# Optimization experiments

Hardware: AMD Instinct MI355X
Metric: run time of the kernel (lower is better)

Reference implementation:

```python
import jax, jax.numpy as jnp
import numpy as np

N_NODES = 100_000
N_EDGES = 1_600_000
N_TRI = 1_000_000
HID = 64
NNZ0 = 2 * N_EDGES  # d0: 2 nonzeros per edge
NNZ1 = 3 * N_TRI    # d1: 3 nonzeros per 2-clique


def spmm(rows, cols, vals, x, n_out):
    """out[r] = sum_{k: rows[k]==r} vals[k] * x[cols[k]]  (sparse @ dense)."""
    return jax.ops.segment_sum(vals[:, None] * x[cols], rows, num_segments=n_out)


def setup_inputs() -> dict:
    key = jax.random.key(0)
    ks = jax.random.split(key, 12)
    q = jax.random.normal(ks[0], (N_NODES, HID), dtype=jnp.float32)
    p = jax.random.normal(ks[1], (N_EDGES, HID), dtype=jnp.float32)
    # attention weights used as divisors -> keep bounded away from 0
    A0 = jax.random.uniform(ks[2], (N_NODES,), jnp.float32, 0.5, 1.5)
    A1 = jax.random.uniform(ks[3], (N_EDGES,), jnp.float32, 0.5, 1.5)
    A2 = jax.random.uniform(ks[4], (N_TRI,), jnp.float32, 0.5, 1.5)
    alpha_raw = jnp.ones((1,), dtype=jnp.float32)
    d0_rows = jax.random.randint(ks[5], (NNZ0,), 0, N_EDGES, dtype=jnp.int32)
    d0_cols = jax.random.randint(ks[6], (NNZ0,), 0, N_NODES, dtype=jnp.int32)
    d0_vals = jax.random.normal(ks[7], (NNZ0,), dtype=jnp.float32)
    d1_rows = jax.random.randint(ks[8], (NNZ1,), 0, N_TRI, dtype=jnp.int32)
    d1_cols = jax.random.randint(ks[9], (NNZ1,), 0, N_EDGES, dtype=jnp.int32)
    d1_vals = jax.random.normal(ks[10], (NNZ1,), dtype=jnp.float32)
    return {
        "q": q, "p": p, "A0": A0, "A1": A1, "A2": A2, "alpha_raw": alpha_raw,
        "d0_rows": d0_rows, "d0_cols": d0_cols, "d0_vals": d0_vals,
        "d1_rows": d1_rows, "d1_cols": d1_cols, "d1_vals": d1_vals,
    }


def reference(q, p, A0, A1, A2, alpha_raw,
              d0_rows, d0_cols, d0_vals, d1_rows, d1_cols, d1_vals):
    n_nodes = q.shape[0]
    n_edges = p.shape[0]
    n_tri = A2.shape[0]
    alpha = jax.nn.sigmoid(alpha_raw)  # opt['alpha_multiplier']
    a0 = A0[:, None]  # [N,1]
    a1 = A1[:, None]  # [E,1]
    a2 = A2[:, None]  # [T,1]

    # bracket == 'gradient'
    # qPart = -alpha * d0^T (A1 * d0 (q / A0)) / A0
    d0ainvq = spmm(d0_rows, d0_cols, d0_vals, q / a0, n_edges)          # [E,H]
    qPart = -alpha * spmm(d0_cols, d0_rows, d0_vals, a1 * d0ainvq, n_nodes) / a0

    # pPart = -alpha * ( d1^T (A2 * d1 (p / A1)) / A1 + d0 (d0^T p / A0) )
    d1ainvp = spmm(d1_rows, d1_cols, d1_vals, p / a1, n_tri)            # [T,H]
    d1ad1Part = spmm(d1_cols, d1_rows, d1_vals, a2 * d1ainvp, n_edges) / a1
    a0invd0tp = spmm(d0_cols, d0_rows, d0_vals, p, n_nodes) / a0        # [N,H]
    d0d0aPart = spmm(d0_rows, d0_cols, d0_vals, a0invd0tp, n_edges)     # [E,H]
    pPart = -alpha * (d1ad1Part + d0d0aPart)

    return (qPart, pPart)
```

## Files before the change

kernel.cpp:

```cpp
#include <hip/hip_runtime.h>

#define HID 64

typedef unsigned short ushort_t;
typedef unsigned int uint_t;
typedef float fx4 __attribute__((ext_vector_type(4)));

__device__ __forceinline__ ushort_t f2bf(float f) {
    uint_t u = __float_as_uint(f);
    u += 0x7FFFu + ((u >> 16) & 1u);
    return (ushort_t)(u >> 16);
}
__device__ __forceinline__ float bf2f(ushort_t h) {
    return __uint_as_float(((uint_t)h) << 16);
}

__device__ __forceinline__ void ntstore4(float* dst, float a, float b, float c, float d) {
    fx4 t; t[0] = a; t[1] = b; t[2] = c; t[3] = d;
    __builtin_nontemporal_store(t, (fx4*)dst);
}


__global__ __launch_bounds__(256) void count_pair(const int* __restrict__ ra,
                                                  const int* __restrict__ rb,
                                                  int* __restrict__ rowcat,
                                                  int offa, int offb, int nnz) {
    int k = blockIdx.x * 256 + threadIdx.x;
    if (k >= nnz) return;
    atomicAdd(&rowcat[offa + ra[k] + 1], 1);
    atomicAdd(&rowcat[offb + rb[k] + 1], 1);
}

__global__ __launch_bounds__(256) void fill_pair(const int* __restrict__ ra,
                                                 const int* __restrict__ rb,
                                                 const float* __restrict__ vals,
                                                 const float* __restrict__ divdiag,
                                                 int* __restrict__ rowcat,
                                                 int offa, int offb,
                                                 int2* __restrict__ pcvcat, int nnz) {
    int k = blockIdx.x * 256 + threadIdx.x;
    if (k >= nnz) return;
    int A = __builtin_nontemporal_load(ra + k);
    int B = __builtin_nontemporal_load(rb + k);
    float v = __builtin_nontemporal_load(vals + k);
    float vd = v / divdiag[B];
    int pa = atomicAdd(&rowcat[offa + A], 1);
    int2 e1; e1.x = B; e1.y = __float_as_int(vd);
    pcvcat[pa] = e1;
    int pb = atomicAdd(&rowcat[offb + B], 1);
    int2 e2; e2.x = A; e2.y = __float_as_int(v);
    pcvcat[pb] = e2;
}

#define SCAN_TPB 256
#define SCAN_IPT 32
#define SCAN_TILE (SCAN_TPB * SCAN_IPT)

__global__ __launch_bounds__(256) void scan1(int* __restrict__ data,
                                             int* __restrict__ blockSums, int n) {
    __shared__ int sdata[SCAN_TPB];
    int base = blockIdx.x * SCAN_TILE + threadIdx.x * SCAN_IPT;
    int v[SCAN_IPT];
    int s = 0;
#pragma unroll
    for (int i = 0; i < SCAN_IPT; ++i) {
        int idx = base + i;
        int x = (idx < n) ? data[idx] : 0;
        s += x;
        v[i] = s;
    }
    sdata[threadIdx.x] = s;
    __syncthreads();
    for (int off = 1; off < SCAN_TPB; off <<= 1) {
        int t = (threadIdx.x >= off) ? sdata[threadIdx.x - off] : 0;
        __syncthreads();
        sdata[threadIdx.x] += t;
        __syncthreads();
    }
    int excl = (threadIdx.x == 0) ? 0 : sdata[threadIdx.x - 1];
#pragma unroll
    for (int i = 0; i < SCAN_IPT; ++i) {
        int idx = base + i;
        if (idx < n) data[idx] = v[i] + excl;
    }
    if (threadIdx.x == SCAN_TPB - 1) blockSums[blockIdx.x] = sdata[SCAN_TPB - 1];
}

__global__ __launch_bounds__(1024) void scan2(int* __restrict__ blockSums, int nb) {
    __shared__ int sdata[1024];
    int x = (threadIdx.x < nb) ? blockSums[threadIdx.x] : 0;
    sdata[threadIdx.x] = x;
    __syncthreads();
    for (int off = 1; off < 1024; off <<= 1) {
        int t = (threadIdx.x >= off) ? sdata[threadIdx.x - off] : 0;
        __syncthreads();
        sdata[threadIdx.x] += t;
        __syncthreads();
    }
    if (threadIdx.x < nb) blockSums[threadIdx.x] = sdata[threadIdx.x];
}

__global__ __launch_bounds__(256) void scan3(int* __restrict__ data,
                                             const int* __restrict__ blockSums, int n) {
    if (blockIdx.x == 0) return;
    int add = blockSums[blockIdx.x - 1];
    int base = blockIdx.x * SCAN_TILE + threadIdx.x;
#pragma unroll
    for (int i = 0; i < SCAN_IPT; ++i) {
        int idx = base + i * SCAN_TPB;
        if (idx < n) data[idx] += add;
    }
}


__global__ __launch_bounds__(256) void f32_to_bf16(const float* __restrict__ src,
                                                   ushort_t* __restrict__ dst, size_t n) {
    size_t i = ((size_t)blockIdx.x * 256 + threadIdx.x) * 4;
    if (i + 3 < n) {
        float4 v = *(const float4*)(src + i);
        ushort4 o;
        o.x = f2bf(v.x); o.y = f2bf(v.y); o.z = f2bf(v.z); o.w = f2bf(v.w);
        *(ushort4*)(dst + i) = o;
    } else {
        for (; i < n; ++i) dst[i] = f2bf(src[i]);
    }
}


template <int SRCH>
__device__ __forceinline__ float4 gather_row(const void* __restrict__ xv, int col, int h4) {
    if constexpr (SRCH) {
        ushort4 hv = *((const ushort4*)((const ushort_t*)xv + (size_t)col * HID) + h4);
        float4 r; r.x = bf2f(hv.x); r.y = bf2f(hv.y); r.z = bf2f(hv.z); r.w = bf2f(hv.w);
        return r;
    } else {
        return *((const float4*)((const float*)xv + (size_t)col * HID) + h4);
    }
}

template <int SRCH, int OUTH>
__global__ __launch_bounds__(256) void csr_spmm4(
    const int* __restrict__ rps, const int2* __restrict__ pcv,
    const void* __restrict__ xv, void* __restrict__ outv,
    const float* __restrict__ rmul, const float* __restrict__ rdiv,
    const float* __restrict__ alpha_raw, int nrows)
{
    int h4 = threadIdx.x & 15;
    int sub16 = threadIdx.x >> 4;
    int rbase = (blockIdx.x * 16 + sub16) * 4;
    if (rbase >= nrows) return;
    int rp[5];
#pragma unroll
    for (int i = 0; i < 5; ++i) rp[i] = rps[min(rbase + i, nrows)];
    int len[4];
#pragma unroll
    for (int r = 0; r < 4; ++r) len[r] = rp[r + 1] - rp[r];
    int maxlen = max(max(len[0], len[1]), max(len[2], len[3]));
    float4 acc[4];
#pragma unroll
    for (int r = 0; r < 4; ++r) acc[r] = float4{0.f, 0.f, 0.f, 0.f};

    for (int j = 0; j < maxlen; ++j) {
#pragma unroll
        for (int r = 0; r < 4; ++r) {
            if (j < len[r]) {
                int2 e = pcv[rp[r] + j];
                float v = __int_as_float(e.y);
                float4 g = gather_row<SRCH>(xv, e.x, h4);
                acc[r].x += v * g.x; acc[r].y += v * g.y;
                acc[r].z += v * g.z; acc[r].w += v * g.w;
            }
        }
    }

    float sgn = alpha_raw ? -(1.0f / (1.0f + expf(-alpha_raw[0]))) : 1.0f;
#pragma unroll
    for (int r = 0; r < 4; ++r) {
        int row = rbase + r;
        if (row >= nrows) break;
        float s = sgn;
        if (rmul) s *= rmul[row];
        if (rdiv) s /= rdiv[row];
        float4 a = acc[r];
        a.x *= s; a.y *= s; a.z *= s; a.w *= s;
        if constexpr (OUTH) {
            ushort4 o;
            o.x = f2bf(a.x); o.y = f2bf(a.y); o.z = f2bf(a.z); o.w = f2bf(a.w);
            *((ushort4*)((ushort_t*)outv + (size_t)row * HID) + h4) = o;
        } else {
            ntstore4((float*)((float4*)((float*)outv + (size_t)row * HID) + h4),
                     a.x, a.y, a.z, a.w);
        }
    }
}

__global__ __launch_bounds__(256) void csr_fused4(
    const int* __restrict__ rpsA, const int* __restrict__ rpsB,
    const int2* __restrict__ pcv,
    const ushort_t* __restrict__ xA, const ushort_t* __restrict__ xB,
    const float* __restrict__ a1d, const float* __restrict__ alpha_raw,
    float* __restrict__ out, int nrows)
{
    int h4 = threadIdx.x & 15;
    int sub16 = threadIdx.x >> 4;
    int rbase = (blockIdx.x * 16 + sub16) * 4;
    if (rbase >= nrows) return;

    int rpA[5], rpB[5];
#pragma unroll
    for (int i = 0; i < 5; ++i) {
        int idx = min(rbase + i, nrows);
        rpA[i] = rpsA[idx];
        rpB[i] = rpsB[idx];
    }
    int lA[4], lB[4];
#pragma unroll
    for (int r = 0; r < 4; ++r) { lA[r] = rpA[r+1] - rpA[r]; lB[r] = rpB[r+1] - rpB[r]; }
    int mA = max(max(lA[0], lA[1]), max(lA[2], lA[3]));
    int mB = max(max(lB[0], lB[1]), max(lB[2], lB[3]));

    float4 accA[4], accB[4];
#pragma unroll
    for (int r = 0; r < 4; ++r) { accA[r] = float4{0,0,0,0}; accB[r] = float4{0,0,0,0}; }

    for (int j = 0; j < mA; ++j) {
#pragma unroll
        for (int r = 0; r < 4; ++r) {
            if (j < lA[r]) {
                int2 e = pcv[rpA[r] + j];
                float v = __int_as_float(e.y);
                ushort4 hv = *((const ushort4*)(xA + (size_t)e.x * HID) + h4);
                accA[r].x += v * bf2f(hv.x); accA[r].y += v * bf2f(hv.y);
                accA[r].z += v * bf2f(hv.z); accA[r].w += v * bf2f(hv.w);
            }
        }
    }
    for (int j = 0; j < mB; ++j) {
#pragma unroll
        for (int r = 0; r < 4; ++r) {
            if (j < lB[r]) {
                int2 e = pcv[rpB[r] + j];
                float v = __int_as_float(e.y);
                ushort4 hv = *((const ushort4*)(xB + (size_t)e.x * HID) + h4);
                accB[r].x += v * bf2f(hv.x); accB[r].y += v * bf2f(hv.y);
                accB[r].z += v * bf2f(hv.z); accB[r].w += v * bf2f(hv.w);
            }
        }
    }

    float ns = -(1.0f / (1.0f + expf(-alpha_raw[0])));
#pragma unroll
    for (int r = 0; r < 4; ++r) {
        int row = rbase + r;
        if (row >= nrows) break;
        float inv_a1 = 1.0f / a1d[row];
        ntstore4((float*)((float4*)(out + (size_t)row * HID) + h4),
                 ns * (accA[r].x + accB[r].x * inv_a1),
                 ns * (accA[r].y + accB[r].y * inv_a1),
                 ns * (accA[r].z + accB[r].z * inv_a1),
                 ns * (accA[r].w + accB[r].w * inv_a1));
    }
}


__global__ __launch_bounds__(256) void count_rows(const int* __restrict__ ridx,
                                                  int* __restrict__ rowptr, int nnz) {
    int k = blockIdx.x * 256 + threadIdx.x;
    if (k < nnz) atomicAdd(&rowptr[ridx[k] + 1], 1);
}

__global__ __launch_bounds__(256) void copy_int(const int* __restrict__ src,
                                                int* __restrict__ dst, int n) {
    int i = blockIdx.x * 256 + threadIdx.x;
    if (i < n) dst[i] = src[i];
}

__global__ __launch_bounds__(256) void fill_csr(const int* __restrict__ ridx,
                                                const int* __restrict__ cidx,
                                                const float* __restrict__ vals,
                                                int* __restrict__ cursor,
                                                int2* __restrict__ pcv, int nnz) {
    int k = blockIdx.x * 256 + threadIdx.x;
    if (k >= nnz) return;
    int pos = atomicAdd(&cursor[ridx[k]], 1);
    int2 e;
    e.x = cidx[k];
    e.y = __float_as_int(vals[k]);
    pcv[pos] = e;
}

template <int SRCH, int OUTH>
__global__ __launch_bounds__(256) void csr_spmm_t(
    const int* __restrict__ rowptr, const int2* __restrict__ pcv,
    const void* __restrict__ xv, void* __restrict__ outv,
    const float* __restrict__ gdiag, int gdiv,
    const float* __restrict__ rmul,
    const float* __restrict__ rdiv,
    const float* __restrict__ alpha_raw,
    int nrows)
{
    int lane = threadIdx.x & 63;
    int wave = threadIdx.x >> 6;
    int sub = lane >> 4;
    int h4 = lane & 15;
    int row = blockIdx.x * 16 + wave * 4 + sub;
    if (row >= nrows) return;
    int start = rowptr[row], end = rowptr[row + 1];
    float4 acc = {0.f, 0.f, 0.f, 0.f};
    for (int j = start; j < end; ++j) {
        int2 e = pcv[j];
        int c = e.x;
        float v = __int_as_float(e.y);
        if (gdiag) { float t = gdiag[c]; v = gdiv ? v / t : v * t; }
        float4 xvv = gather_row<SRCH>(xv, c, h4);
        acc.x += v * xvv.x; acc.y += v * xvv.y; acc.z += v * xvv.z; acc.w += v * xvv.w;
    }
    float s = 1.0f;
    if (rmul) s *= rmul[row];
    if (rdiv) s /= rdiv[row];
    if (alpha_raw) s *= -(1.0f / (1.0f + expf(-alpha_raw[0])));
    acc.x *= s; acc.y *= s; acc.z *= s; acc.w *= s;
    if constexpr (OUTH) {
        ushort_t* out = (ushort_t*)outv;
        ushort4 o;
        o.x = f2bf(acc.x); o.y = f2bf(acc.y); o.z = f2bf(acc.z); o.w = f2bf(acc.w);
        *((ushort4*)(out + (size_t)row * HID) + h4) = o;
    } else {
        float* out = (float*)outv;
        *((float4*)(out + (size_t)row * HID) + h4) = acc;
    }
}

template <int BH>
__global__ __launch_bounds__(256) void csr_spmm_fused_t(
    const int* __restrict__ rowptrA, const int2* __restrict__ pcvA, const float* __restrict__ xA,
    const int* __restrict__ rowptrB, const int2* __restrict__ pcvB, const void* __restrict__ xBv,
    const float* __restrict__ a1, const float* __restrict__ alpha_raw,
    float* __restrict__ out, int nrows)
{
    int lane = threadIdx.x & 63;
    int wave = threadIdx.x >> 6;
    int sub = lane >> 4;
    int h4 = lane & 15;
    int row = blockIdx.x * 16 + wave * 4 + sub;
    if (row >= nrows) return;

    float4 accA = {0.f, 0.f, 0.f, 0.f};
    {
        int start = rowptrA[row], end = rowptrA[row + 1];
        for (int j = start; j < end; ++j) {
            int2 e = pcvA[j];
            float v = __int_as_float(e.y);
            const float4 xv = *((const float4*)(xA + (size_t)e.x * HID) + h4);
            accA.x += v * xv.x; accA.y += v * xv.y; accA.z += v * xv.z; accA.w += v * xv.w;
        }
    }
    float4 accB = {0.f, 0.f, 0.f, 0.f};
    {
        int start = rowptrB[row], end = rowptrB[row + 1];
        for (int j = start; j < end; ++j) {
            int2 e = pcvB[j];
            float v = __int_as_float(e.y);
            float4 xv = gather_row<BH>(xBv, e.x, h4);
            accB.x += v * xv.x; accB.y += v * xv.y; accB.z += v * xv.z; accB.w += v * xv.w;
        }
    }
    float inv_a1 = 1.0f / a1[row];
    float ns = -(1.0f / (1.0f + expf(-alpha_raw[0])));
    float4 r;
    r.x = ns * (accA.x + accB.x * inv_a1);
    r.y = ns * (accA.y + accB.y * inv_a1);
    r.z = ns * (accA.z + accB.z * inv_a1);
    r.w = ns * (accA.w + accB.w * inv_a1);
    *((float4*)(out + (size_t)row * HID) + h4) = r;
}

__global__ __launch_bounds__(256) void spmm_scatter(
    const int* __restrict__ gidx, const int* __restrict__ sidx,
    const float* __restrict__ vals, const float* __restrict__ x,
    float* __restrict__ out,
    const float* __restrict__ gscale, int ginv,
    const float* __restrict__ sscale, int sinv,
    const float* __restrict__ alpha_raw, int nnz)
{
    int k = (blockIdx.x << 2) | (threadIdx.x >> 6);
    if (k >= nnz) return;
    int h = threadIdx.x & 63;
    int g = gidx[k];
    int s = sidx[k];
    float f = vals[k];
    if (gscale) { float t = gscale[g]; f = ginv ? (f / t) : (f * t); }
    if (sscale) { float t = sscale[s]; f = sinv ? (f / t) : (f * t); }
    if (alpha_raw) {
        float sig = 1.0f / (1.0f + expf(-alpha_raw[0]));
        f = -f * sig;
    }
    atomicAdd(out + (size_t)s * HID + h, f * x[(size_t)g * HID + h]);
}


extern "C" void kernel_launch(void* const* d_in, const int* in_sizes, int n_in,
                              void* d_out, int out_size, void* d_ws, size_t ws_size,
                              hipStream_t stream) {
    const float* q         = (const float*)d_in[0];
    const float* p         = (const float*)d_in[1];
    const float* A0        = (const float*)d_in[2];
    const float* A1        = (const float*)d_in[3];
    const float* A2        = (const float*)d_in[4];
    const float* alpha_raw = (const float*)d_in[5];
    const int*   d0_rows   = (const int*)d_in[6];
    const int*   d0_cols   = (const int*)d_in[7];
    const float* d0_vals   = (const float*)d_in[8];
    const int*   d1_rows   = (const int*)d_in[9];
    const int*   d1_cols   = (const int*)d_in[10];
    const float* d1_vals   = (const float*)d_in[11];

    const int n_nodes = in_sizes[2];
    const int n_edges = in_sizes[3];
    const int n_tri   = in_sizes[4];
    const int nnz0    = in_sizes[6];
    const int nnz1    = in_sizes[9];

    float* qPart = (float*)d_out;
    float* pPart = (float*)d_out + (size_t)n_nodes * HID;

    const size_t qPartBytes = (size_t)n_nodes * HID * sizeof(float);
    const size_t pPartBytes = (size_t)n_edges * HID * sizeof(float);

    dim3 blk(256);

    const int off_d0r = 0;
    const int off_d0c = off_d0r + n_edges;
    const int off_d1r = off_d0c + n_nodes;
    const int off_d1c = off_d1r + n_tri;
    const int NR      = off_d1c + n_edges;

    {
        char* w = (char*)d_ws;
        auto alloc = [&](size_t bytes) -> char* {
            char* ptr = w;
            w += (bytes + 255) & ~(size_t)255;
            return ptr;
        };
        ushort_t* bufA   = (ushort_t*)alloc((size_t)n_edges * HID * sizeof(ushort_t));
        ushort_t* tmp_th = (ushort_t*)alloc((size_t)n_tri * HID * sizeof(ushort_t));
        ushort_t* tmp_nh = (ushort_t*)alloc((size_t)n_nodes * HID * sizeof(ushort_t));
        int*      Z      = (int*)alloc((size_t)(NR + 2) * sizeof(int));
        int*      rowcat = Z + 1;
        int*      blockSums = (int*)alloc(2048 * sizeof(int));
        int2*     pcvcat = (int2*)alloc(((size_t)nnz0 * 2 + (size_t)nnz1 * 2) * sizeof(int2));
        size_t needed = (size_t)(w - (char*)d_ws);

        if (needed <= ws_size) {
            hipMemsetAsync(Z, 0, (size_t)(NR + 2) * sizeof(int), stream);
            dim3 gk0((nnz0 + 255) / 256);
            dim3 gk1((nnz1 + 255) / 256);
            count_pair<<<gk0, blk, 0, stream>>>(d0_rows, d0_cols, rowcat, off_d0r, off_d0c, nnz0);
            count_pair<<<gk1, blk, 0, stream>>>(d1_rows, d1_cols, rowcat, off_d1r, off_d1c, nnz1);
            {
                int n = NR + 1;
                int nb = (n + SCAN_TILE - 1) / SCAN_TILE;
                scan1<<<nb, SCAN_TPB, 0, stream>>>(rowcat, blockSums, n);
                scan2<<<1, 1024, 0, stream>>>(blockSums, nb);
                scan3<<<nb, SCAN_TPB, 0, stream>>>(rowcat, blockSums, n);
            }
            fill_pair<<<gk0, blk, 0, stream>>>(d0_rows, d0_cols, d0_vals, A0,
                                               rowcat, off_d0r, off_d0c, pcvcat, nnz0);
            fill_pair<<<gk1, blk, 0, stream>>>(d1_rows, d1_cols, d1_vals, A1,
                                               rowcat, off_d1r, off_d1c, pcvcat, nnz1);

            size_t np = (size_t)n_edges * HID;
            f32_to_bf16<<<(unsigned)((np / 4 + 255) / 256), blk, 0, stream>>>(p, bufA, np);

            csr_spmm4<1, 1><<<(n_tri + 63) / 64, blk, 0, stream>>>(
                Z + off_d1r, pcvcat, bufA, tmp_th, A2, nullptr, nullptr, n_tri);

            csr_spmm4<1, 1><<<(n_nodes + 63) / 64, blk, 0, stream>>>(
                Z + off_d0c, pcvcat, bufA, tmp_nh, nullptr, nullptr, nullptr, n_nodes);

            csr_spmm4<0, 1><<<(n_edges + 63) / 64, blk, 0, stream>>>(
                Z + off_d0r, pcvcat, q, bufA, A1, nullptr, nullptr, n_edges);

            csr_spmm4<1, 0><<<(n_nodes + 63) / 64, blk, 0, stream>>>(
                Z + off_d0c, pcvcat, bufA, qPart, nullptr, A0, alpha_raw, n_nodes);

            csr_fused4<<<(n_edges + 63) / 64, blk, 0, stream>>>(
                Z + off_d0r, Z + off_d1c, pcvcat, tmp_nh, tmp_th,
                A1, alpha_raw, pPart, n_edges);
            return;
        }
    }

    {
        char* w = (char*)d_ws;
        auto alloc = [&](size_t bytes) -> char* {
            char* ptr = w;
            w += (bytes + 255) & ~(size_t)255;
            return ptr;
        };
        float* tmp_t = (float*)alloc((size_t)n_tri * HID * sizeof(float));
        float* tmp_n = (float*)alloc((size_t)n_nodes * HID * sizeof(float));
        size_t rpTotal = (size_t)(n_edges + 1) + (n_nodes + 1) + (n_tri + 1) + (n_edges + 1);
        int* rpBase = (int*)alloc(rpTotal * sizeof(int));
        int* rp_d0r = rpBase;
        int* rp_d0c = rp_d0r + (n_edges + 1);
        int* rp_d1r = rp_d0c + (n_nodes + 1);
        int* rp_d1c = rp_d1r + (n_tri + 1);
        int nmax = n_edges > n_tri ? n_edges : n_tri;
        if (n_nodes > nmax) nmax = n_nodes;
        int* cursor    = (int*)alloc((size_t)nmax * sizeof(int));
        int* blockSums = (int*)alloc(2048 * sizeof(int));
        int2* pcv_d0r = (int2*)alloc((size_t)nnz0 * sizeof(int2));
        int2* pcv_d0c = (int2*)alloc((size_t)nnz0 * sizeof(int2));
        int2* pcv_d1r = (int2*)alloc((size_t)nnz1 * sizeof(int2));
        int2* pcv_d1c = (int2*)alloc((size_t)nnz1 * sizeof(int2));
        size_t needed = (size_t)(w - (char*)d_ws);

        if (needed <= ws_size) {
            hipMemsetAsync(rpBase, 0, rpTotal * sizeof(int), stream);
            dim3 gk0((nnz0 + 255) / 256);
            dim3 gk1((nnz1 + 255) / 256);
            count_rows<<<gk0, blk, 0, stream>>>(d0_rows, rp_d0r, nnz0);
            count_rows<<<gk0, blk, 0, stream>>>(d0_cols, rp_d0c, nnz0);
            count_rows<<<gk1, blk, 0, stream>>>(d1_rows, rp_d1r, nnz1);
            count_rows<<<gk1, blk, 0, stream>>>(d1_cols, rp_d1c, nnz1);

            struct Build {
                int* rowptr; int nout; const int* ridx; const int* cidx; const float* vals;
                int2* pcv; int nnz;
            } builds[4] = {
                { rp_d0r, n_edges, d0_rows, d0_cols, d0_vals, pcv_d0r, nnz0 },
                { rp_d0c, n_nodes, d0_cols, d0_rows, d0_vals, pcv_d0c, nnz0 },
                { rp_d1r, n_tri,   d1_rows, d1_cols, d1_vals, pcv_d1r, nnz1 },
                { rp_d1c, n_edges, d1_cols, d1_rows, d1_vals, pcv_d1c, nnz1 },
            };
            for (int b = 0; b < 4; ++b) {
                int n = builds[b].nout + 1;
                int nb = (n + SCAN_TILE - 1) / SCAN_TILE;
                scan1<<<nb, SCAN_TPB, 0, stream>>>(builds[b].rowptr, blockSums, n);
                scan2<<<1, 1024, 0, stream>>>(blockSums, nb);
                scan3<<<nb, SCAN_TPB, 0, stream>>>(builds[b].rowptr, blockSums, n);
                copy_int<<<(builds[b].nout + 255) / 256, blk, 0, stream>>>(
                    builds[b].rowptr, cursor, builds[b].nout);
                fill_csr<<<(builds[b].nnz + 255) / 256, blk, 0, stream>>>(
                    builds[b].ridx, builds[b].cidx, builds[b].vals, cursor,
                    builds[b].pcv, builds[b].nnz);
            }

            float* tmp_e1 = pPart;
            csr_spmm_t<0, 0><<<(n_edges + 15) / 16, blk, 0, stream>>>(
                rp_d0r, pcv_d0r, q, tmp_e1, A0, 1, A1, nullptr, nullptr, n_edges);
            csr_spmm_t<0, 0><<<(n_nodes + 15) / 16, blk, 0, stream>>>(
                rp_d0c, pcv_d0c, tmp_e1, qPart, nullptr, 0, nullptr, A0, alpha_raw, n_nodes);
            csr_spmm_t<0, 0><<<(n_tri + 15) / 16, blk, 0, stream>>>(
                rp_d1r, pcv_d1r, p, tmp_t, A1, 1, A2, nullptr, nullptr, n_tri);
            csr_spmm_t<0, 0><<<(n_nodes + 15) / 16, blk, 0, stream>>>(
                rp_d0c, pcv_d0c, p, tmp_n, nullptr, 0, nullptr, A0, nullptr, n_nodes);
            csr_spmm_fused_t<0><<<(n_edges + 15) / 16, blk, 0, stream>>>(
                rp_d0r, pcv_d0r, tmp_n,
                rp_d1c, pcv_d1c, tmp_t,
                A1, alpha_raw, pPart, n_edges);
            return;
        }
    }

    {
        float* tmp = (float*)d_ws;
        const size_t triBytes  = (size_t)n_tri * HID * sizeof(float);
        const size_t nodeBytes = qPartBytes;
        dim3 g0((nnz0 + 3) / 4);
        dim3 g1((nnz1 + 3) / 4);
        hipMemsetAsync(qPart, 0, qPartBytes, stream);
        hipMemsetAsync(pPart, 0, pPartBytes, stream);
        spmm_scatter<<<g0, blk, 0, stream>>>(d0_cols, d0_rows, d0_vals, q, pPart,
                                             A0, 1, nullptr, 0, nullptr, nnz0);
        spmm_scatter<<<g0, blk, 0, stream>>>(d0_rows, d0_cols, d0_vals, pPart, qPart,
                                             A1, 0, A0, 1, alpha_raw, nnz0);
        hipMemsetAsync(pPart, 0, pPartBytes, stream);
        hipMemsetAsync(tmp, 0, triBytes, stream);
        spmm_scatter<<<g1, blk, 0, stream>>>(d1_cols, d1_rows, d1_vals, p, tmp,
                                             A1, 1, nullptr, 0, nullptr, nnz1);
        spmm_scatter<<<g1, blk, 0, stream>>>(d1_rows, d1_cols, d1_vals, tmp, pPart,
                                             A2, 0, A1, 1, alpha_raw, nnz1);
        hipMemsetAsync(tmp, 0, nodeBytes, stream);
        spmm_scatter<<<g0, blk, 0, stream>>>(d0_rows, d0_cols, d0_vals, p, tmp,
                                             nullptr, 0, A0, 1, nullptr, nnz0);
        spmm_scatter<<<g0, blk, 0, stream>>>(d0_cols, d0_rows, d0_vals, tmp, pPart,
                                             nullptr, 0, nullptr, 0, alpha_raw, nnz0);
    }
}
```

Baseline: 2.375 ms.

## Fuse CSR build passes and spmm stages, record atomic ranks to drop fill atomics

The count pass now records each nonzero's rank from the atomic counter, so the fill pass can place entries without a second round of atomics. The fill pass is merged with the fp32-to-bf16 conversion of p, with fill and convert blocks interleaved. The two spmm stages that read p are merged into one launch. The q-path edge spmm is fused into the final pPart kernel because both walk the same d0-row CSR. Gather loops are unrolled by two with clamped indices so loads are issued early. Ranks are stored as 16-bit values, which assumes no row has more than 65535 entries, and the rank buffer reuses tmp_th.

```diff
diff --git a/kernel.cpp b/kernel.cpp
--- a/kernel.cpp
+++ b/kernel.cpp
@@ -4,6 +4,7 @@
 
 typedef unsigned short ushort_t;
 typedef unsigned int uint_t;
+typedef unsigned long long ull_t;
 typedef float fx4 __attribute__((ext_vector_type(4)));
 
 __device__ __forceinline__ ushort_t f2bf(float f) {
@@ -20,36 +21,106 @@
     __builtin_nontemporal_store(t, (fx4*)dst);
 }
 
-
-__global__ __launch_bounds__(256) void count_pair(const int* __restrict__ ra,
-                                                  const int* __restrict__ rb,
-                                                  int* __restrict__ rowcat,
-                                                  int offa, int offb, int nnz) {
-    int k = blockIdx.x * 256 + threadIdx.x;
-    if (k >= nnz) return;
-    atomicAdd(&rowcat[offa + ra[k] + 1], 1);
-    atomicAdd(&rowcat[offb + rb[k] + 1], 1);
-}
-
-__global__ __launch_bounds__(256) void fill_pair(const int* __restrict__ ra,
-                                                 const int* __restrict__ rb,
-                                                 const float* __restrict__ vals,
-                                                 const float* __restrict__ divdiag,
-                                                 int* __restrict__ rowcat,
-                                                 int offa, int offb,
-                                                 int2* __restrict__ pcvcat, int nnz) {
-    int k = blockIdx.x * 256 + threadIdx.x;
-    if (k >= nnz) return;
-    int A = __builtin_nontemporal_load(ra + k);
-    int B = __builtin_nontemporal_load(rb + k);
-    float v = __builtin_nontemporal_load(vals + k);
-    float vd = v / divdiag[B];
-    int pa = atomicAdd(&rowcat[offa + A], 1);
-    int2 e1; e1.x = B; e1.y = __float_as_int(vd);
-    pcvcat[pa] = e1;
-    int pb = atomicAdd(&rowcat[offb + B], 1);
-    int2 e2; e2.x = A; e2.y = __float_as_int(v);
-    pcvcat[pb] = e2;
+__device__ __forceinline__ ull_t packCV(int col, float v) {
+    return ((ull_t)(uint_t)__float_as_int(v) << 32) | (uint_t)col;
+}
+
+
+__global__ __launch_bounds__(256) void count_rank2(
+    const int* __restrict__ d0r, const int* __restrict__ d0c,
+    const int* __restrict__ d1r, const int* __restrict__ d1c,
+    int* __restrict__ rowcat,
+    ushort2* __restrict__ rank0, ushort2* __restrict__ rank1,
+    int off_d0r, int off_d0c, int off_d1r, int off_d1c,
+    int nnz0, int nnz1)
+{
+    int b = blockIdx.x;
+    int cb0 = (nnz0 + 255) >> 8;
+    if (b < cb0) {
+        int k = b * 256 + threadIdx.x;
+        if (k < nnz0) {
+            int A = d0r[k], B = d0c[k];
+            int r0 = atomicAdd(&rowcat[off_d0r + A + 1], 1);
+            int r1 = atomicAdd(&rowcat[off_d0c + B + 1], 1);
+            ushort2 rk; rk.x = (unsigned short)r0; rk.y = (unsigned short)r1;
+            rank0[k] = rk;
+        }
+    } else {
+        int k = (b - cb0) * 256 + threadIdx.x;
+        if (k < nnz1) {
+            int A = d1r[k], B = d1c[k];
+            int r0 = atomicAdd(&rowcat[off_d1r + A + 1], 1);
+            int r1 = atomicAdd(&rowcat[off_d1c + B + 1], 1);
+            ushort2 rk; rk.x = (unsigned short)r0; rk.y = (unsigned short)r1;
+            rank1[k] = rk;
+        }
+    }
+}
+
+__global__ __launch_bounds__(256) void fill_conv(
+    const int* __restrict__ d0r, const int* __restrict__ d0c,
+    const float* __restrict__ v0, const float* __restrict__ A0d,
+    const int* __restrict__ d1r, const int* __restrict__ d1c,
+    const float* __restrict__ v1, const float* __restrict__ A1d,
+    const int* __restrict__ S,
+    const ushort2* __restrict__ rank0, const ushort2* __restrict__ rank1,
+    ull_t* __restrict__ pcv,
+    int off_d0r, int off_d0c, int off_d1r, int off_d1c,
+    int nnz0, int nnz1,
+    const float* __restrict__ p, ushort_t* __restrict__ ph, long long np,
+    int nfill, int npair)
+{
+    int b = blockIdx.x;
+    int fb = -1, vb = -1;
+    if (b < 2 * npair) {
+        if (b & 1) vb = b >> 1; else fb = b >> 1;
+    } else {
+        int rem = b - 2 * npair;
+        if (nfill > npair) fb = npair + rem; else vb = npair + rem;
+    }
+    if (fb >= 0) {
+        int cb0 = (nnz0 + 255) >> 8;
+        if (fb < cb0) {
+            int k = fb * 256 + threadIdx.x;
+            if (k < nnz0) {
+                int A = __builtin_nontemporal_load(d0r + k);
+                int B = __builtin_nontemporal_load(d0c + k);
+                float v = __builtin_nontemporal_load(v0 + k);
+                ushort2 rk = rank0[k];
+                __builtin_nontemporal_store(packCV(B, v / A0d[B]),
+                                            &pcv[S[off_d0r + A] + rk.x]);
+                __builtin_nontemporal_store(packCV(A, v),
+                                            &pcv[S[off_d0c + B] + rk.y]);
+            }
+        } else {
+            int k = (fb - cb0) * 256 + threadIdx.x;
+            if (k < nnz1) {
+                int A = __builtin_nontemporal_load(d1r + k);
+                int B = __builtin_nontemporal_load(d1c + k);
+                float v = __builtin_nontemporal_load(v1 + k);
+                ushort2 rk = rank1[k];
+                __builtin_nontemporal_store(packCV(B, v / A1d[B]),
+                                            &pcv[S[off_d1r + A] + rk.x]);
+                __builtin_nontemporal_store(packCV(A, v),
+                                            &pcv[S[off_d1c + B] + rk.y]);
+            }
+        }
+    } else {
+        const fx4* p4 = (const fx4*)p;
+        ushort4* h4p = (ushort4*)ph;
+        long long nf4 = np >> 2;
+        long long f0 = (long long)vb * 1024 + threadIdx.x;
+#pragma unroll
+        for (int c = 0; c < 4; ++c) {
+            long long f = f0 + c * 256;
+            if (f < nf4) {
+                fx4 v = __builtin_nontemporal_load(p4 + f);
+                ushort4 o;
+                o.x = f2bf(v[0]); o.y = f2bf(v[1]); o.z = f2bf(v[2]); o.w = f2bf(v[3]);
+                h4p[f] = o;
+            }
+        }
+    }
 }
 
 #define SCAN_TPB 256
@@ -113,20 +184,6 @@
 }
 
 
-__global__ __launch_bounds__(256) void f32_to_bf16(const float* __restrict__ src,
-                                                   ushort_t* __restrict__ dst, size_t n) {
-    size_t i = ((size_t)blockIdx.x * 256 + threadIdx.x) * 4;
-    if (i + 3 < n) {
-        float4 v = *(const float4*)(src + i);
-        ushort4 o;
-        o.x = f2bf(v.x); o.y = f2bf(v.y); o.z = f2bf(v.z); o.w = f2bf(v.w);
-        *(ushort4*)(dst + i) = o;
-    } else {
-        for (; i < n; ++i) dst[i] = f2bf(src[i]);
-    }
-}
-
-
 template <int SRCH>
 __device__ __forceinline__ float4 gather_row(const void* __restrict__ xv, int col, int h4) {
     if constexpr (SRCH) {
@@ -139,37 +196,50 @@
 }
 
 template <int SRCH, int OUTH>
-__global__ __launch_bounds__(256) void csr_spmm4(
+__device__ __forceinline__ void spmm4_body(
     const int* __restrict__ rps, const int2* __restrict__ pcv,
     const void* __restrict__ xv, void* __restrict__ outv,
     const float* __restrict__ rmul, const float* __restrict__ rdiv,
-    const float* __restrict__ alpha_raw, int nrows)
+    const float* __restrict__ alpha_raw, int nrows, int blk)
 {
     int h4 = threadIdx.x & 15;
     int sub16 = threadIdx.x >> 4;
-    int rbase = (blockIdx.x * 16 + sub16) * 4;
+    int rbase = (blk * 16 + sub16) * 4;
     if (rbase >= nrows) return;
     int rp[5];
 #pragma unroll
     for (int i = 0; i < 5; ++i) rp[i] = rps[min(rbase + i, nrows)];
-    int len[4];
-#pragma unroll
-    for (int r = 0; r < 4; ++r) len[r] = rp[r + 1] - rp[r];
+    int len[4], last[4];
+#pragma unroll
+    for (int r = 0; r < 4; ++r) {
+        len[r] = rp[r + 1] - rp[r];
+        last[r] = max(rp[r + 1] - 1, 0);
+    }
     int maxlen = max(max(len[0], len[1]), max(len[2], len[3]));
     float4 acc[4];
 #pragma unroll
     for (int r = 0; r < 4; ++r) acc[r] = float4{0.f, 0.f, 0.f, 0.f};
 
-    for (int j = 0; j < maxlen; ++j) {
+    for (int j = 0; j < maxlen; j += 2) {
+        int2 e0[4], e1[4];
 #pragma unroll
         for (int r = 0; r < 4; ++r) {
-            if (j < len[r]) {
-                int2 e = pcv[rp[r] + j];
-                float v = __int_as_float(e.y);
-                float4 g = gather_row<SRCH>(xv, e.x, h4);
-                acc[r].x += v * g.x; acc[r].y += v * g.y;
-                acc[r].z += v * g.z; acc[r].w += v * g.w;
-            }
+            e0[r] = pcv[min(rp[r] + j, last[r])];
+            e1[r] = pcv[min(rp[r] + j + 1, last[r])];
+        }
+        float4 g0[4], g1[4];
+#pragma unroll
+        for (int r = 0; r < 4; ++r) g0[r] = gather_row<SRCH>(xv, e0[r].x, h4);
+#pragma unroll
+        for (int r = 0; r < 4; ++r) g1[r] = gather_row<SRCH>(xv, e1[r].x, h4);
+#pragma unroll
+        for (int r = 0; r < 4; ++r) {
+            float va = (j < len[r]) ? __int_as_float(e0[r].y) : 0.f;
+            float vb = (j + 1 < len[r]) ? __int_as_float(e1[r].y) : 0.f;
+            acc[r].x += va * g0[r].x + vb * g1[r].x;
+            acc[r].y += va * g0[r].y + vb * g1[r].y;
+            acc[r].z += va * g0[r].z + vb * g1[r].z;
+            acc[r].w += va * g0[r].w + vb * g1[r].w;
         }
     }
 
@@ -194,12 +264,36 @@
     }
 }
 
-__global__ __launch_bounds__(256) void csr_fused4(
+template <int SRCH, int OUTH>
+__global__ __launch_bounds__(256) void csr_spmm4(
+    const int* __restrict__ rps, const int2* __restrict__ pcv,
+    const void* __restrict__ xv, void* __restrict__ outv,
+    const float* __restrict__ rmul, const float* __restrict__ rdiv,
+    const float* __restrict__ alpha_raw, int nrows)
+{
+    spmm4_body<SRCH, OUTH>(rps, pcv, xv, outv, rmul, rdiv, alpha_raw, nrows, blockIdx.x);
+}
+
+__global__ __launch_bounds__(256) void csr_spmm_dual(
+    const int* __restrict__ rpsT, const int* __restrict__ rpsN,
+    const int2* __restrict__ pcv, const ushort_t* __restrict__ ph,
+    ushort_t* __restrict__ outT, ushort_t* __restrict__ outN,
+    const float* __restrict__ a2, int n_tri, int n_nodes, int triBlocks)
+{
+    if ((int)blockIdx.x < triBlocks)
+        spmm4_body<1, 1>(rpsT, pcv, ph, outT, a2, nullptr, nullptr, n_tri, blockIdx.x);
+    else
+        spmm4_body<1, 1>(rpsN, pcv, ph, outN, nullptr, nullptr, nullptr, n_nodes,
+                         blockIdx.x - triBlocks);
+}
+
+__global__ __launch_bounds__(256) void csr_fused_epq(
     const int* __restrict__ rpsA, const int* __restrict__ rpsB,
     const int2* __restrict__ pcv,
-    const ushort_t* __restrict__ xA, const ushort_t* __restrict__ xB,
+    const float* __restrict__ q, const ushort_t* __restrict__ tmpn,
+    const ushort_t* __restrict__ tmpt,
     const float* __restrict__ a1d, const float* __restrict__ alpha_raw,
-    float* __restrict__ out, int nrows)
+    ushort_t* __restrict__ oute1, float* __restrict__ outp, int nrows)
 {
     int h4 = threadIdx.x & 15;
     int sub16 = threadIdx.x >> 4;
@@ -213,38 +307,66 @@
         rpA[i] = rpsA[idx];
         rpB[i] = rpsB[idx];
     }
-    int lA[4], lB[4];
-#pragma unroll
-    for (int r = 0; r < 4; ++r) { lA[r] = rpA[r+1] - rpA[r]; lB[r] = rpB[r+1] - rpB[r]; }
+    int lA[4], lastA[4], lB[4], lastB[4];
+#pragma unroll
+    for (int r = 0; r < 4; ++r) {
+        lA[r] = rpA[r + 1] - rpA[r]; lastA[r] = max(rpA[r + 1] - 1, 0);
+        lB[r] = rpB[r + 1] - rpB[r]; lastB[r] = max(rpB[r + 1] - 1, 0);
+    }
     int mA = max(max(lA[0], lA[1]), max(lA[2], lA[3]));
     int mB = max(max(lB[0], lB[1]), max(lB[2], lB[3]));
 
-    float4 accA[4], accB[4];
-#pragma unroll
-    for (int r = 0; r < 4; ++r) { accA[r] = float4{0,0,0,0}; accB[r] = float4{0,0,0,0}; }
+    float4 accQ[4], accN[4], accT[4];
+#pragma unroll
+    for (int r = 0; r < 4; ++r) {
+        accQ[r] = float4{0.f, 0.f, 0.f, 0.f};
+        accN[r] = float4{0.f, 0.f, 0.f, 0.f};
+        accT[r] = float4{0.f, 0.f, 0.f, 0.f};
+    }
 
     for (int j = 0; j < mA; ++j) {
+        int2 e[4];
+#pragma unroll
+        for (int r = 0; r < 4; ++r) e[r] = pcv[min(rpA[r] + j, lastA[r])];
+        float4 gq[4]; ushort4 gn[4];
+#pragma unroll
+        for (int r = 0; r < 4; ++r)
+            gq[r] = *((const float4*)(q + (size_t)e[r].x * HID) + h4);
+#pragma unroll
+        for (int r = 0; r < 4; ++r)
+            gn[r] = *((const ushort4*)(tmpn + (size_t)e[r].x * HID) + h4);
 #pragma unroll
         for (int r = 0; r < 4; ++r) {
-            if (j < lA[r]) {
-                int2 e = pcv[rpA[r] + j];
-                float v = __int_as_float(e.y);
-                ushort4 hv = *((const ushort4*)(xA + (size_t)e.x * HID) + h4);
-                accA[r].x += v * bf2f(hv.x); accA[r].y += v * bf2f(hv.y);
-                accA[r].z += v * bf2f(hv.z); accA[r].w += v * bf2f(hv.w);
-            }
-        }
-    }
-    for (int j = 0; j < mB; ++j) {
+            float v = (j < lA[r]) ? __int_as_float(e[r].y) : 0.f;
+            accQ[r].x += v * gq[r].x; accQ[r].y += v * gq[r].y;
+            accQ[r].z += v * gq[r].z; accQ[r].w += v * gq[r].w;
+            accN[r].x += v * bf2f(gn[r].x); accN[r].y += v * bf2f(gn[r].y);
+            accN[r].z += v * bf2f(gn[r].z); accN[r].w += v * bf2f(gn[r].w);
+        }
+    }
+
+    for (int j = 0; j < mB; j += 2) {
+        int2 e0[4], e1[4];
 #pragma unroll
         for (int r = 0; r < 4; ++r) {
-            if (j < lB[r]) {
-                int2 e = pcv[rpB[r] + j];
-                float v = __int_as_float(e.y);
-                ushort4 hv = *((const ushort4*)(xB + (size_t)e.x * HID) + h4);
-                accB[r].x += v * bf2f(hv.x); accB[r].y += v * bf2f(hv.y);
-                accB[r].z += v * bf2f(hv.z); accB[r].w += v * bf2f(hv.w);
-            }
+            e0[r] = pcv[min(rpB[r] + j, lastB[r])];
+            e1[r] = pcv[min(rpB[r] + j + 1, lastB[r])];
+        }
+        ushort4 g0[4], g1[4];
+#pragma unroll
+        for (int r = 0; r < 4; ++r)
+            g0[r] = *((const ushort4*)(tmpt + (size_t)e0[r].x * HID) + h4);
+#pragma unroll
+        for (int r = 0; r < 4; ++r)
+            g1[r] = *((const ushort4*)(tmpt + (size_t)e1[r].x * HID) + h4);
+#pragma unroll
+        for (int r = 0; r < 4; ++r) {
+            float va = (j < lB[r]) ? __int_as_float(e0[r].y) : 0.f;
+            float vb = (j + 1 < lB[r]) ? __int_as_float(e1[r].y) : 0.f;
+            accT[r].x += va * bf2f(g0[r].x) + vb * bf2f(g1[r].x);
+            accT[r].y += va * bf2f(g0[r].y) + vb * bf2f(g1[r].y);
+            accT[r].z += va * bf2f(g0[r].z) + vb * bf2f(g1[r].z);
+            accT[r].w += va * bf2f(g0[r].w) + vb * bf2f(g1[r].w);
         }
     }
 
@@ -253,12 +375,17 @@
     for (int r = 0; r < 4; ++r) {
         int row = rbase + r;
         if (row >= nrows) break;
-        float inv_a1 = 1.0f / a1d[row];
-        ntstore4((float*)((float4*)(out + (size_t)row * HID) + h4),
-                 ns * (accA[r].x + accB[r].x * inv_a1),
-                 ns * (accA[r].y + accB[r].y * inv_a1),
-                 ns * (accA[r].z + accB[r].z * inv_a1),
-                 ns * (accA[r].w + accB[r].w * inv_a1));
+        float a1v = a1d[row];
+        ushort4 o;
+        o.x = f2bf(accQ[r].x * a1v); o.y = f2bf(accQ[r].y * a1v);
+        o.z = f2bf(accQ[r].z * a1v); o.w = f2bf(accQ[r].w * a1v);
+        *((ushort4*)(oute1 + (size_t)row * HID) + h4) = o;
+        float ia = 1.0f / a1v;
+        ntstore4((float*)((float4*)(outp + (size_t)row * HID) + h4),
+                 ns * (accN[r].x + accT[r].x * ia),
+                 ns * (accN[r].y + accT[r].y * ia),
+                 ns * (accN[r].z + accT[r].z * ia),
+                 ns * (accN[r].w + accT[r].w * ia));
     }
 }
 
@@ -446,47 +573,57 @@
         ushort_t* tmp_th = (ushort_t*)alloc((size_t)n_tri * HID * sizeof(ushort_t));
         ushort_t* tmp_nh = (ushort_t*)alloc((size_t)n_nodes * HID * sizeof(ushort_t));
         int*      Z      = (int*)alloc((size_t)(NR + 2) * sizeof(int));
-        int*      rowcat = Z + 1;
+        int*      S      = Z + 1;
         int*      blockSums = (int*)alloc(2048 * sizeof(int));
         int2*     pcvcat = (int2*)alloc(((size_t)nnz0 * 2 + (size_t)nnz1 * 2) * sizeof(int2));
+        size_t rankBytes = ((size_t)nnz0 + (size_t)nnz1) * sizeof(ushort2);
+        ushort2* rank0;
+        if (rankBytes <= (size_t)n_tri * HID * sizeof(ushort_t))
+            rank0 = (ushort2*)tmp_th;
+        else
+            rank0 = (ushort2*)alloc(rankBytes);
+        ushort2* rank1 = rank0 + nnz0;
         size_t needed = (size_t)(w - (char*)d_ws);
 
         if (needed <= ws_size) {
             hipMemsetAsync(Z, 0, (size_t)(NR + 2) * sizeof(int), stream);
-            dim3 gk0((nnz0 + 255) / 256);
-            dim3 gk1((nnz1 + 255) / 256);
-            count_pair<<<gk0, blk, 0, stream>>>(d0_rows, d0_cols, rowcat, off_d0r, off_d0c, nnz0);
-            count_pair<<<gk1, blk, 0, stream>>>(d1_rows, d1_cols, rowcat, off_d1r, off_d1c, nnz1);
+            int cb0 = (nnz0 + 255) / 256;
+            int cb1 = (nnz1 + 255) / 256;
+            count_rank2<<<cb0 + cb1, blk, 0, stream>>>(
+                d0_rows, d0_cols, d1_rows, d1_cols, S, rank0, rank1,
+                off_d0r, off_d0c, off_d1r, off_d1c, nnz0, nnz1);
             {
                 int n = NR + 1;
                 int nb = (n + SCAN_TILE - 1) / SCAN_TILE;
-                scan1<<<nb, SCAN_TPB, 0, stream>>>(rowcat, blockSums, n);
+                scan1<<<nb, SCAN_TPB, 0, stream>>>(S, blockSums, n);
                 scan2<<<1, 1024, 0, stream>>>(blockSums, nb);
-                scan3<<<nb, SCAN_TPB, 0, stream>>>(rowcat, blockSums, n);
+                scan3<<<nb, SCAN_TPB, 0, stream>>>(S, blockSums, n);
             }
-            fill_pair<<<gk0, blk, 0, stream>>>(d0_rows, d0_cols, d0_vals, A0,
-                                               rowcat, off_d0r, off_d0c, pcvcat, nnz0);
-            fill_pair<<<gk1, blk, 0, stream>>>(d1_rows, d1_cols, d1_vals, A1,
-                                               rowcat, off_d1r, off_d1c, pcvcat, nnz1);
-
-            size_t np = (size_t)n_edges * HID;
-            f32_to_bf16<<<(unsigned)((np / 4 + 255) / 256), blk, 0, stream>>>(p, bufA, np);
-
-            csr_spmm4<1, 1><<<(n_tri + 63) / 64, blk, 0, stream>>>(
-                Z + off_d1r, pcvcat, bufA, tmp_th, A2, nullptr, nullptr, n_tri);
-
-            csr_spmm4<1, 1><<<(n_nodes + 63) / 64, blk, 0, stream>>>(
-                Z + off_d0c, pcvcat, bufA, tmp_nh, nullptr, nullptr, nullptr, n_nodes);
-
-            csr_spmm4<0, 1><<<(n_edges + 63) / 64, blk, 0, stream>>>(
-                Z + off_d0r, pcvcat, q, bufA, A1, nullptr, nullptr, n_edges);
-
-            csr_spmm4<1, 0><<<(n_nodes + 63) / 64, blk, 0, stream>>>(
-                Z + off_d0c, pcvcat, bufA, qPart, nullptr, A0, alpha_raw, n_nodes);
-
-            csr_fused4<<<(n_edges + 63) / 64, blk, 0, stream>>>(
-                Z + off_d0r, Z + off_d1c, pcvcat, tmp_nh, tmp_th,
-                A1, alpha_raw, pPart, n_edges);
+            long long np = (long long)n_edges * HID;
+            int cbc = (int)((np / 4 + 1023) / 1024);
+            int nfill = cb0 + cb1;
+            int npair = min(nfill, cbc);
+            fill_conv<<<nfill + cbc, blk, 0, stream>>>(
+                d0_rows, d0_cols, d0_vals, A0,
+                d1_rows, d1_cols, d1_vals, A1,
+                S, rank0, rank1, (ull_t*)pcvcat,
+                off_d0r, off_d0c, off_d1r, off_d1c, nnz0, nnz1,
+                p, bufA, np, nfill, npair);
+
+            int triB  = (n_tri + 63) / 64;
+            int nodeB = (n_nodes + 63) / 64;
+            int edgeB = (n_edges + 63) / 64;
+
+            csr_spmm_dual<<<triB + nodeB, blk, 0, stream>>>(
+                S + off_d1r, S + off_d0c, pcvcat, bufA, tmp_th, tmp_nh,
+                A2, n_tri, n_nodes, triB);
+
+            csr_fused_epq<<<edgeB, blk, 0, stream>>>(
+                S + off_d0r, S + off_d1c, pcvcat, q, tmp_nh, tmp_th,
+                A1, alpha_raw, bufA, pPart, n_edges);
+
+            csr_spmm4<1, 0><<<nodeB, blk, 0, stream>>>(
+                S + off_d0c, pcvcat, bufA, qPart, nullptr, A0, alpha_raw, n_nodes);
             return;
         }
     }
```

After: 2.021 ms. 14.9% less time.
